# Kernel tuning notes

Hardware: AMD Instinct MI355X
Metric: run time of the kernel (lower is better)

The kernel has to match this reference:

```python
import jax, jax.numpy as jnp
import numpy as np

N_NODES = 50000
N_EDGES = 1600000
IN_CH = 512
HID = 8      # per-head features, layer 1
HEADS = 8
OUT_CH = 40  # num classes
NEG_SLOPE = 0.2  # PyG GATConv default leaky_relu slope


def setup_inputs() -> dict:
    key = jax.random.key(0)
    ks = jax.random.split(key, 8)
    x = jax.random.uniform(ks[0], (N_NODES, IN_CH), dtype=jnp.float32)
    edge_index = jax.random.randint(ks[1], (2, N_EDGES), 0, N_NODES, dtype=jnp.int64)
    s1 = 1.0 / np.sqrt(IN_CH)
    s2 = 1.0 / np.sqrt(HEADS * HID)
    W1 = jax.random.normal(ks[2], (IN_CH, HEADS * HID), dtype=jnp.float32) * s1
    att_src1 = jax.random.normal(ks[3], (HEADS, HID), dtype=jnp.float32) * s2
    att_dst1 = jax.random.normal(ks[4], (HEADS, HID), dtype=jnp.float32) * s2
    b1 = jnp.zeros((HEADS * HID,), dtype=jnp.float32)
    W2 = jax.random.normal(ks[5], (HEADS * HID, OUT_CH), dtype=jnp.float32) * s2
    att_src2 = jax.random.normal(ks[6], (1, OUT_CH), dtype=jnp.float32) * 0.15
    att_dst2 = jax.random.normal(ks[7], (1, OUT_CH), dtype=jnp.float32) * 0.15
    b2 = jnp.zeros((OUT_CH,), dtype=jnp.float32)
    return {"x": x, "edge_index": edge_index, "W1": W1, "att_src1": att_src1,
            "att_dst1": att_dst1, "b1": b1, "W2": W2, "att_src2": att_src2,
            "att_dst2": att_dst2, "b2": b2}


def _row_normalize(x):
    return x / jnp.clip(x.sum(axis=1, keepdims=True), 1e-8, None)


def _gat_conv(x, src, dst, W, att_src, att_dst, bias, heads, out_ch, concat):
    """PyG GATConv (self-loops already included in src/dst)."""
    n = x.shape[0]
    h = (x @ W).reshape(n, heads, out_ch)          # [N, H, C]
    a_src = jnp.sum(h * att_src, axis=-1)          # [N, H]
    a_dst = jnp.sum(h * att_dst, axis=-1)          # [N, H]
    alpha = jax.nn.leaky_relu(a_src[src] + a_dst[dst], NEG_SLOPE)  # [E, H]
    # segment softmax over incoming edges of each dst node
    m = jax.ops.segment_max(alpha, dst, num_segments=n)            # [N, H]
    e = jnp.exp(alpha - m[dst])
    denom = jax.ops.segment_sum(e, dst, num_segments=n)            # [N, H]
    alpha = e / (denom[dst] + 1e-16)
    msg = h[src] * alpha[:, :, None]               # [E, H, C]
    out = jax.ops.segment_sum(msg, dst, num_segments=n)            # [N, H, C]
    out = out.reshape(n, heads * out_ch) if concat else out.mean(axis=1)
    return out + bias


def reference(x, edge_index, W1, att_src1, att_dst1, b1, W2, att_src2, att_dst2, b2):
    n = x.shape[0]
    loops = jnp.arange(n, dtype=edge_index.dtype)
    src = jnp.concatenate([edge_index[0], loops])
    dst = jnp.concatenate([edge_index[1], loops])
    h = _row_normalize(x)
    # dropout omitted: inference mode (training=False)
    h = jax.nn.elu(_gat_conv(h, src, dst, W1, att_src1, att_dst1, b1, HEADS, HID, True))
    return _gat_conv(h, src, dst, W2, att_src2, att_dst2, b2, 1, OUT_CH, False)
```

## Files before the change

### kernel.cpp

```cpp
#include <hip/hip_runtime.h>
#include <math.h>

#define N_NODES 50000
#define IN_CH   512
#define HID     8
#define HEADS   8
#define C1      64
#define OUT_CH  40
#define NEG_SLOPE 0.2f
#define NB      ((N_NODES + 255) / 256)
#define TILE    4096
#define CAP     16384
#define PACKW_BLOCKS 128
#define GEMM1_BLOCKS ((N_NODES + 31) / 32)

__device__ __forceinline__ float leaky(float v) { return fmaxf(v, NEG_SLOPE * v); }
__device__ __forceinline__ float fexp(float v) { return __expf(v); }

typedef __attribute__((ext_vector_type(8))) short short8;
typedef __attribute__((ext_vector_type(4))) short short4v;
typedef __attribute__((ext_vector_type(4))) float f32x4;

__device__ __forceinline__ unsigned short f2bf(float f) {
    unsigned u = __builtin_bit_cast(unsigned, f);
    u += 0x7FFFu + ((u >> 16) & 1u);
    return (unsigned short)(u >> 16);
}
__device__ __forceinline__ float bf2f(unsigned short h) {
    unsigned u = ((unsigned)h) << 16;
    return __builtin_bit_cast(float, u);
}

#define XH_STRIDE_B 272

__global__ __launch_bounds__(256) void k_pre(
    const float* __restrict__ W1, short* __restrict__ bph, short* __restrict__ bpl,
    const int* __restrict__ src, const int* __restrict__ dst, int E,
    int* __restrict__ coarseCur, unsigned int* __restrict__ pairs)
{
    __shared__ int  hist[256];
    __shared__ int  scn[256];
    __shared__ int  offs[256];
    __shared__ unsigned int  pairBuf[TILE];
    __shared__ unsigned char bktBuf[TILE];

    const int t = threadIdx.x;

    if (blockIdx.x < PACKW_BLOCKS) {
        const int idx = blockIdx.x * 256 + t;
        const int k = idx >> 6, col = idx & 63;
        const float w = W1[idx];
        const unsigned short hi = f2bf(w);
        const unsigned short lo = f2bf(w - bf2f(hi));
        const int di = ((k >> 5) * 64 + col) * 32 + (k & 31);
        bph[di] = (short)hi;
        bpl[di] = (short)lo;
        return;
    }

    const int tileBase = (blockIdx.x - PACKW_BLOCKS) * TILE;
    const int n = min(TILE, E - tileBase);

    hist[t] = 0;
    __syncthreads();

    for (int e = t; e < n; e += 256)
        atomicAdd(&hist[dst[tileBase + e] >> 8], 1);
    __syncthreads();

    scn[t] = hist[t];
    __syncthreads();
    #pragma unroll
    for (int off = 1; off < 256; off <<= 1) {
        int xv = (t >= off) ? scn[t - off] : 0;
        __syncthreads();
        scn[t] += xv;
        __syncthreads();
    }

    {
        const int h  = hist[t];
        const int ls = scn[t] - h;
        int off = 0;
        if (h > 0) {
            const int gbase = t * CAP + atomicAdd(&coarseCur[t], h);
            off = gbase - ls;
        }
        offs[t] = off;
        hist[t] = ls;
    }
    __syncthreads();

    for (int e = t; e < n; e += 256) {
        const int s = src[tileBase + e];
        const int d = dst[tileBase + e];
        const int bkt = d >> 8;
        const int pos = atomicAdd(&hist[bkt], 1);
        pairBuf[pos] = (unsigned)s | ((unsigned)(d & 255) << 17);
        bktBuf[pos]  = (unsigned char)bkt;
    }
    __syncthreads();

    for (int i = t; i < n; i += 256)
        pairs[i + offs[bktBuf[i]]] = pairBuf[i];
}

__global__ __launch_bounds__(256) void k_mid(
    const float* __restrict__ x,
    const short* __restrict__ bph, const short* __restrict__ bpl,
    const float* __restrict__ attS, const float* __restrict__ attD,
    unsigned short* __restrict__ h1b, float* __restrict__ aS, float* __restrict__ aD,
    const int* __restrict__ coarseCur, const unsigned int* __restrict__ pairs,
    int* __restrict__ ssrc, int* __restrict__ cumS, int* __restrict__ cumE)
{
    __shared__ unsigned char smem[17536];

    const int tid = threadIdx.x;

    if (blockIdx.x >= GEMM1_BLOCKS) {
        int* hist = (int*)smem;
        int* scn  = hist + 256;
        int* cur  = scn + 256;
        const int b = blockIdx.x - GEMM1_BLOCKS;
        const int t = tid;
        const int dbase = b << 8;
        const int nd = min(256, N_NODES - dbase);
        const int lo = b * CAP;
        const int hi = lo + coarseCur[b];

        hist[t] = 0;
        __syncthreads();
        for (int j = lo + t; j < hi; j += 256)
            atomicAdd(&hist[(pairs[j] >> 17) & 255], 1);
        __syncthreads();

        const int hv = hist[t];
        scn[t] = hv;
        __syncthreads();
        #pragma unroll
        for (int off = 1; off < 256; off <<= 1) {
            int xv = (t >= off) ? scn[t - off] : 0;
            __syncthreads();
            scn[t] += xv;
            __syncthreads();
        }
        if (t < nd) {
            cumS[dbase + t] = lo + scn[t] - hv;
            cumE[dbase + t] = lo + scn[t];
        }
        cur[t] = lo + scn[t] - hv;
        __syncthreads();

        for (int j = lo + t; j < hi; j += 256) {
            const unsigned int p = pairs[j];
            const int pos = atomicAdd(&cur[(p >> 17) & 255], 1);
            ssrc[pos] = (int)(p & 0x1FFFFu);
        }
        return;
    }

    short* xh = (short*)smem;
    short* xl = (short*)(smem + 8704);
    float* rowsum = (float*)(smem + 17408);
    float* houtf  = (float*)smem;

    const int lane = tid & 63;
    const int w    = tid >> 6;
    const int row_off = (w & 1) * 16;
    const int col_off = (w >> 1) * 32;
    const int rowBase = blockIdx.x * 32;

    const int l15 = lane & 15;
    const int kg  = lane >> 4;
    const int a_base = (l15 + row_off) * XH_STRIDE_B + kg * 16;

    const int srow = tid >> 5;
    const int sk4  = tid & 31;

    f32x4 acc0 = {0.f, 0.f, 0.f, 0.f};
    f32x4 acc1 = {0.f, 0.f, 0.f, 0.f};
    float psum[4] = {0.f, 0.f, 0.f, 0.f};
    float4 va[4], vb[4];

    auto LOAD = [&](int c, float4 (&v)[4]) {
        #pragma unroll
        for (int i = 0; i < 4; ++i) {
            const int grow = rowBase + i * 8 + srow;
            v[i] = (grow < N_NODES)
                 ? *(const float4*)(x + (size_t)grow * IN_CH + c * 128 + sk4 * 4)
                 : make_float4(0.f, 0.f, 0.f, 0.f);
        }
    };
    auto STAGE = [&](float4 (&v)[4]) {
        #pragma unroll
        for (int i = 0; i < 4; ++i) {
            const int row = i * 8 + srow;
            const unsigned short h0 = f2bf(v[i].x), h1u = f2bf(v[i].y),
                                 h2 = f2bf(v[i].z), h3  = f2bf(v[i].w);
            short4v hvv = { (short)h0, (short)h1u, (short)h2, (short)h3 };
            short4v lvv = { (short)f2bf(v[i].x - bf2f(h0)), (short)f2bf(v[i].y - bf2f(h1u)),
                            (short)f2bf(v[i].z - bf2f(h2)), (short)f2bf(v[i].w - bf2f(h3)) };
            *(short4v*)((char*)xh + row * XH_STRIDE_B + sk4 * 8) = hvv;
            *(short4v*)((char*)xl + row * XH_STRIDE_B + sk4 * 8) = lvv;
            psum[i] += v[i].x + v[i].y + v[i].z + v[i].w;
        }
    };
    auto MFMA = [&](int c) {
        #pragma unroll
        for (int kk2 = 0; kk2 < 4; ++kk2) {
            const int kk = c * 4 + kk2;
            const short8 ah = *(const short8*)((const char*)xh + a_base + kk2 * 64);
            const short8 al = *(const short8*)((const char*)xl + a_base + kk2 * 64);
            const int b0 = (kk * 64 + col_off + l15) * 32 + kg * 8;
            const int b1 = b0 + 16 * 32;
            const short8 bh0 = *(const short8*)(bph + b0);
            const short8 bl0 = *(const short8*)(bpl + b0);
            const short8 bh1 = *(const short8*)(bph + b1);
            const short8 bl1 = *(const short8*)(bpl + b1);
            acc0 = __builtin_amdgcn_mfma_f32_16x16x32_bf16(ah, bh0, acc0, 0, 0, 0);
            acc1 = __builtin_amdgcn_mfma_f32_16x16x32_bf16(ah, bh1, acc1, 0, 0, 0);
            acc0 = __builtin_amdgcn_mfma_f32_16x16x32_bf16(ah, bl0, acc0, 0, 0, 0);
            acc1 = __builtin_amdgcn_mfma_f32_16x16x32_bf16(ah, bl1, acc1, 0, 0, 0);
            acc0 = __builtin_amdgcn_mfma_f32_16x16x32_bf16(al, bh0, acc0, 0, 0, 0);
            acc1 = __builtin_amdgcn_mfma_f32_16x16x32_bf16(al, bh1, acc1, 0, 0, 0);
        }
    };

    LOAD(0, va);
    STAGE(va);
    __syncthreads();
    LOAD(1, vb);
    MFMA(0);
    __syncthreads();
    STAGE(vb);
    __syncthreads();
    LOAD(2, va);
    MFMA(1);
    __syncthreads();
    STAGE(va);
    __syncthreads();
    LOAD(3, vb);
    MFMA(2);
    __syncthreads();
    STAGE(vb);
    #pragma unroll
    for (int i = 0; i < 4; ++i) {
        float s = psum[i];
        #pragma unroll
        for (int off = 16; off; off >>= 1) s += __shfl_xor(s, off, 32);
        if (sk4 == 0) rowsum[i * 8 + srow] = s;
    }
    __syncthreads();
    MFMA(3);
    __syncthreads();

    #pragma unroll
    for (int r = 0; r < 4; ++r) {
        const int row = row_off + kg * 4 + r;
        const float rs = fmaxf(rowsum[row], 1e-8f);
        houtf[row * 68 + col_off + l15]      = acc0[r] / rs;
        houtf[row * 68 + col_off + 16 + l15] = acc1[r] / rs;
    }
    __syncthreads();

    #pragma unroll
    for (int i = tid; i < 32 * 16; i += 256) {
        const int row = i >> 4, seg = i & 15;
        if (rowBase + row < N_NODES) {
            const float* hs = houtf + row * 68 + seg * 4;
            short4v o = { (short)f2bf(hs[0]), (short)f2bf(hs[1]),
                          (short)f2bf(hs[2]), (short)f2bf(hs[3]) };
            *(short4v*)(h1b + (size_t)(rowBase + row) * 64 + seg * 4) = o;
        }
    }

    {
        const int row = tid >> 3, hd = tid & 7;
        if (rowBase + row < N_NODES) {
            float vs = 0.f, vd = 0.f;
            #pragma unroll
            for (int e2 = 0; e2 < 8; ++e2) {
                const float hv = houtf[row * 68 + hd * 8 + e2];
                vs = fmaf(hv, attS[hd * 8 + e2], vs);
                vd = fmaf(hv, attD[hd * 8 + e2], vd);
            }
            aS[(size_t)(rowBase + row) * 8 + hd] = vs;
            aD[(size_t)(rowBase + row) * 8 + hd] = vd;
        }
    }
}

__global__ __launch_bounds__(256) void k_agg1f(
    const int* __restrict__ cumS, const int* __restrict__ cumE,
    const int* __restrict__ ssrc,
    const float* __restrict__ aS, const float* __restrict__ aD,
    const unsigned short* __restrict__ h1b, const float* __restrict__ b1,
    const float* __restrict__ W2,
    const float* __restrict__ attS2, const float* __restrict__ attD2,
    unsigned short* __restrict__ h2b, float* __restrict__ a2s, float* __restrict__ a2d)
{
    __shared__ float w2s[64 * 40];
    __shared__ float hstage[4][64];

    const int tid  = threadIdx.x;
    const int lane = tid & 63;
    const int w    = tid >> 6;
    const int node = __builtin_amdgcn_readfirstlane(blockIdx.x * 4 + w);
    const int e = lane >> 3;
    const int c = lane & 7;

    #pragma unroll
    for (int i = tid; i < 640; i += 256)
        ((float4*)w2s)[i] = ((const float4*)W2)[i];

    const int start = cumS[node];
    const int end   = cumE[node];

    const float aDn = aD[(size_t)node * 8 + c];
    float acc[8] = {0.f, 0.f, 0.f, 0.f, 0.f, 0.f, 0.f, 0.f};
    float den = 0.f;

    if (e == 0) {
        const float e0 = fexp(leaky(aS[(size_t)node * 8 + c] + aDn));
        const short8 hv = *(const short8*)(h1b + (size_t)node * 64 + c * 8);
        #pragma unroll
        for (int j = 0; j < 8; ++j)
            acc[j] = e0 * bf2f((unsigned short)hv[j]);
        den = e0;
    }

    int base = start;
    for (; base + 32 <= end; base += 32) {
        const int s0 = ssrc[base + e];
        const int s1 = ssrc[base + 8 + e];
        const int s2 = ssrc[base + 16 + e];
        const int s3 = ssrc[base + 24 + e];
        const float aa0 = aS[(size_t)s0 * 8 + c];
        const float aa1 = aS[(size_t)s1 * 8 + c];
        const float aa2 = aS[(size_t)s2 * 8 + c];
        const float aa3 = aS[(size_t)s3 * 8 + c];
        const short8 h0 = *(const short8*)(h1b + ((size_t)s0 << 6) + c * 8);
        const short8 h1v = *(const short8*)(h1b + ((size_t)s1 << 6) + c * 8);
        const short8 h2v = *(const short8*)(h1b + ((size_t)s2 << 6) + c * 8);
        const short8 h3v = *(const short8*)(h1b + ((size_t)s3 << 6) + c * 8);
        const float w0 = fexp(leaky(aa0 + aDn));
        const float w1 = fexp(leaky(aa1 + aDn));
        const float w2 = fexp(leaky(aa2 + aDn));
        const float w3 = fexp(leaky(aa3 + aDn));
        #pragma unroll
        for (int j = 0; j < 8; ++j) {
            acc[j] = fmaf(w0, bf2f((unsigned short)h0[j]), acc[j]);
            acc[j] = fmaf(w1, bf2f((unsigned short)h1v[j]), acc[j]);
            acc[j] = fmaf(w2, bf2f((unsigned short)h2v[j]), acc[j]);
            acc[j] = fmaf(w3, bf2f((unsigned short)h3v[j]), acc[j]);
        }
        den += w0 + w1 + w2 + w3;
    }
    for (; base + 8 <= end; base += 8) {
        const int s = ssrc[base + e];
        const float aa = aS[(size_t)s * 8 + c];
        const short8 hv = *(const short8*)(h1b + ((size_t)s << 6) + c * 8);
        const float wv = fexp(leaky(aa + aDn));
        #pragma unroll
        for (int j = 0; j < 8; ++j)
            acc[j] = fmaf(wv, bf2f((unsigned short)hv[j]), acc[j]);
        den += wv;
    }
    if (base < end) {
        const int nb  = end - base;
        const int idx = base + (e < nb ? e : nb - 1);
        const int s   = ssrc[idx];
        float wv = fexp(leaky(aS[(size_t)s * 8 + c] + aDn));
        if (e >= nb) wv = 0.f;
        const short8 hv = *(const short8*)(h1b + ((size_t)s << 6) + c * 8);
        #pragma unroll
        for (int j = 0; j < 8; ++j)
            acc[j] = fmaf(wv, bf2f((unsigned short)hv[j]), acc[j]);
        den += wv;
    }

    #pragma unroll
    for (int m = 8; m < 64; m <<= 1) {
        den += __shfl_xor(den, m, 64);
        #pragma unroll
        for (int j = 0; j < 8; ++j)
            acc[j] += __shfl_xor(acc[j], m, 64);
    }

    if (e == 0) {
        const float dinv = 1.f / (den + 1e-16f);
        #pragma unroll
        for (int j = 0; j < 8; ++j) {
            const float v = acc[j] * dinv + b1[c * 8 + j];
            hstage[w][c * 8 + j] = v > 0.f ? v : (__expf(v) - 1.f);
        }
    }
    __syncthreads();

    const int j = lane;
    float acc2 = 0.f;
    if (j < OUT_CH) {
        #pragma unroll
        for (int k = 0; k < 64; ++k)
            acc2 = fmaf(hstage[w][k], w2s[k * 40 + j], acc2);
    }
    float vs = (j < OUT_CH) ? acc2 * attS2[j] : 0.f;
    float vd = (j < OUT_CH) ? acc2 * attD2[j] : 0.f;
    #pragma unroll
    for (int off = 32; off; off >>= 1) {
        vs += __shfl_xor(vs, off, 64);
        vd += __shfl_xor(vd, off, 64);
    }
    if (j < OUT_CH) h2b[(size_t)node * 40 + j] = f2bf(acc2);
    if (j == 0) {
        a2s[node] = vs;
        a2d[node] = vd;
    }
}

__global__ __launch_bounds__(256) void k_agg2(
    const int* __restrict__ cumS, const int* __restrict__ cumE,
    const int* __restrict__ ssrc,
    const float* __restrict__ a2s, const float* __restrict__ a2d,
    const unsigned short* __restrict__ h2b, const float* __restrict__ b2,
    float* __restrict__ out)
{
    const int lane = threadIdx.x & 63;
    const int node = __builtin_amdgcn_readfirstlane(blockIdx.x * 4 + (threadIdx.x >> 6));
    const int e = lane >> 3;
    const int c = lane & 7;

    const int start = cumS[node];
    const int end   = cumE[node];

    const float aDd = a2d[node];
    float acc[8] = {0.f, 0.f, 0.f, 0.f, 0.f, 0.f, 0.f, 0.f};
    float den = 0.f;

    if (e == 0) {
        const float e0 = fexp(leaky(a2s[node] + aDd));
        const short8 hv = *(const short8*)(h2b + (size_t)node * 40 + c * 8);
        #pragma unroll
        for (int j = 0; j < 8; ++j)
            acc[j] = e0 * bf2f((unsigned short)hv[j]);
        den = e0;
    }

    int base = start;
    for (; base + 32 <= end; base += 32) {
        const int s0 = ssrc[base + e];
        const int s1 = ssrc[base + 8 + e];
        const int s2 = ssrc[base + 16 + e];
        const int s3 = ssrc[base + 24 + e];
        const float aa0 = a2s[s0];
        const float aa1 = a2s[s1];
        const float aa2 = a2s[s2];
        const float aa3 = a2s[s3];
        const short8 h0 = *(const short8*)(h2b + (size_t)s0 * 40 + c * 8);
        const short8 h1v = *(const short8*)(h2b + (size_t)s1 * 40 + c * 8);
        const short8 h2v = *(const short8*)(h2b + (size_t)s2 * 40 + c * 8);
        const short8 h3v = *(const short8*)(h2b + (size_t)s3 * 40 + c * 8);
        const float w0 = fexp(leaky(aa0 + aDd));
        const float w1 = fexp(leaky(aa1 + aDd));
        const float w2 = fexp(leaky(aa2 + aDd));
        const float w3 = fexp(leaky(aa3 + aDd));
        #pragma unroll
        for (int j = 0; j < 8; ++j) {
            acc[j] = fmaf(w0, bf2f((unsigned short)h0[j]), acc[j]);
            acc[j] = fmaf(w1, bf2f((unsigned short)h1v[j]), acc[j]);
            acc[j] = fmaf(w2, bf2f((unsigned short)h2v[j]), acc[j]);
            acc[j] = fmaf(w3, bf2f((unsigned short)h3v[j]), acc[j]);
        }
        den += w0 + w1 + w2 + w3;
    }
    for (; base + 8 <= end; base += 8) {
        const int s = ssrc[base + e];
        const float aa = a2s[s];
        const short8 hv = *(const short8*)(h2b + (size_t)s * 40 + c * 8);
        const float wv = fexp(leaky(aa + aDd));
        #pragma unroll
        for (int j = 0; j < 8; ++j)
            acc[j] = fmaf(wv, bf2f((unsigned short)hv[j]), acc[j]);
        den += wv;
    }
    if (base < end) {
        const int nb  = end - base;
        const int idx = base + (e < nb ? e : nb - 1);
        const int s   = ssrc[idx];
        float wv = fexp(leaky(a2s[s] + aDd));
        if (e >= nb) wv = 0.f;
        const short8 hv = *(const short8*)(h2b + (size_t)s * 40 + c * 8);
        #pragma unroll
        for (int j = 0; j < 8; ++j)
            acc[j] = fmaf(wv, bf2f((unsigned short)hv[j]), acc[j]);
        den += wv;
    }

    #pragma unroll
    for (int m = 8; m < 64; m <<= 1) {
        den += __shfl_xor(den, m, 64);
        #pragma unroll
        for (int j = 0; j < 8; ++j)
            acc[j] += __shfl_xor(acc[j], m, 64);
    }

    if (e == 0 && c < 5) {
        const float dinv = 1.f / (den + 1e-16f);
        float o[8];
        #pragma unroll
        for (int j = 0; j < 8; ++j)
            o[j] = acc[j] * dinv + b2[c * 8 + j];
        float4* dst0 = (float4*)(out + (size_t)node * OUT_CH + c * 8);
        dst0[0] = make_float4(o[0], o[1], o[2], o[3]);
        dst0[1] = make_float4(o[4], o[5], o[6], o[7]);
    }
}

extern "C" void kernel_launch(void* const* d_in, const int* in_sizes, int n_in,
                              void* d_out, int out_size, void* d_ws, size_t ws_size,
                              hipStream_t stream)
{
    const float* x     = (const float*)d_in[0];
    const int*   ei    = (const int*)d_in[1];
    const float* W1    = (const float*)d_in[2];
    const float* attS1 = (const float*)d_in[3];
    const float* attD1 = (const float*)d_in[4];
    const float* b1    = (const float*)d_in[5];
    const float* W2    = (const float*)d_in[6];
    const float* attS2 = (const float*)d_in[7];
    const float* attD2 = (const float*)d_in[8];
    const float* b2    = (const float*)d_in[9];

    const int E = in_sizes[1] / 2;
    const int* src = ei;
    const int* dst = ei + E;

    float* out = (float*)d_out;
    float* f = (float*)d_ws;
    float* aS1  = f;  f += (size_t)N_NODES * 8;
    float* aD1  = f;  f += (size_t)N_NODES * 8;
    float* a2s  = f;  f += (size_t)N_NODES;
    float* a2d  = f;  f += (size_t)N_NODES;
    unsigned short* h1b = (unsigned short*)f;  f += (size_t)N_NODES * 32;
    unsigned short* h2b = (unsigned short*)f;  f += (size_t)N_NODES * 20 + 64;
    short* bph = (short*)f;  f += 16384;
    short* bpl = (short*)f;  f += 16384;
    unsigned int* pairs = (unsigned int*)f;  f += (size_t)NB * CAP;
    int* ip = (int*)f;
    int* coarseCur = ip;  ip += 256;
    int* cumS      = ip;  ip += N_NODES;
    int* cumE      = ip;  ip += N_NODES;
    int* ssrc      = ip;  ip += (size_t)NB * CAP;

    const int partBlocks = (E + TILE - 1) / TILE;

    hipMemsetAsync(coarseCur, 0, 256 * sizeof(int), stream);

    k_pre<<<PACKW_BLOCKS + partBlocks, 256, 0, stream>>>(W1, bph, bpl,
                                                         src, dst, E, coarseCur, pairs);

    k_mid<<<GEMM1_BLOCKS + NB, 256, 0, stream>>>(x, bph, bpl, attS1, attD1,
                                                 h1b, aS1, aD1,
                                                 coarseCur, pairs, ssrc, cumS, cumE);

    k_agg1f<<<N_NODES / 4, 256, 0, stream>>>(cumS, cumE, ssrc, aS1, aD1, h1b, b1,
                                             W2, attS2, attD2, h2b, a2s, a2d);

    k_agg2<<<N_NODES / 4, 256, 0, stream>>>(cumS, cumE, ssrc, a2s, a2d, h2b, b2, out);
}
```

Before: 171.3 us.

## Load GEMM1 A-operand directly from global into MFMA registers, drop LDS staging

The first-layer GEMM no longer stages x through shared memory as split bf16 hi/lo tiles. Each lane now reads its own 8 contiguous floats per k-step straight from global memory, converts them to hi/lo bf16 in registers and feeds the MFMAs directly. Row sums are reduced with cross-lane shuffles. This removes the LDS writes, LDS reads and several block barriers, and shrinks shared memory use. In exchange, the global loads are 32-byte per-lane strided reads across rows, which coalesce less well than the old row-contiguous float4 pattern, and the software double-buffering is replaced by a plain unrolled loop.

```diff
diff --git a/kernel.cpp b/kernel.cpp
--- a/kernel.cpp
+++ b/kernel.cpp
@@ -31,8 +31,6 @@
     return __builtin_bit_cast(float, u);
 }
 
-#define XH_STRIDE_B 272
-
 __global__ __launch_bounds__(256) void k_pre(
     const float* __restrict__ W1, short* __restrict__ bph, short* __restrict__ bpl,
     const int* __restrict__ src, const int* __restrict__ dst, int E,
@@ -113,12 +111,12 @@
     const int* __restrict__ coarseCur, const unsigned int* __restrict__ pairs,
     int* __restrict__ ssrc, int* __restrict__ cumS, int* __restrict__ cumE)
 {
-    __shared__ unsigned char smem[17536];
+    __shared__ float smemf[32 * 68];
 
     const int tid = threadIdx.x;
 
     if (blockIdx.x >= GEMM1_BLOCKS) {
-        int* hist = (int*)smem;
+        int* hist = (int*)smemf;
         int* scn  = hist + 256;
         int* cur  = scn + 256;
         const int b = blockIdx.x - GEMM1_BLOCKS;
@@ -159,10 +157,7 @@
         return;
     }
 
-    short* xh = (short*)smem;
-    short* xl = (short*)(smem + 8704);
-    float* rowsum = (float*)(smem + 17408);
-    float* houtf  = (float*)smem;
+    float* houtf = smemf;
 
     const int lane = tid & 63;
     const int w    = tid >> 6;
@@ -172,92 +167,53 @@
 
     const int l15 = lane & 15;
     const int kg  = lane >> 4;
-    const int a_base = (l15 + row_off) * XH_STRIDE_B + kg * 16;
-
-    const int srow = tid >> 5;
-    const int sk4  = tid & 31;
+
+    const int myRow = rowBase + row_off + l15;
+    const bool rowOK = (myRow < N_NODES);
+    const float* xrow = x + (size_t)(rowOK ? myRow : 0) * IN_CH + kg * 8;
 
     f32x4 acc0 = {0.f, 0.f, 0.f, 0.f};
     f32x4 acc1 = {0.f, 0.f, 0.f, 0.f};
-    float psum[4] = {0.f, 0.f, 0.f, 0.f};
-    float4 va[4], vb[4];
-
-    auto LOAD = [&](int c, float4 (&v)[4]) {
-        #pragma unroll
-        for (int i = 0; i < 4; ++i) {
-            const int grow = rowBase + i * 8 + srow;
-            v[i] = (grow < N_NODES)
-                 ? *(const float4*)(x + (size_t)grow * IN_CH + c * 128 + sk4 * 4)
-                 : make_float4(0.f, 0.f, 0.f, 0.f);
-        }
-    };
-    auto STAGE = [&](float4 (&v)[4]) {
-        #pragma unroll
-        for (int i = 0; i < 4; ++i) {
-            const int row = i * 8 + srow;
-            const unsigned short h0 = f2bf(v[i].x), h1u = f2bf(v[i].y),
-                                 h2 = f2bf(v[i].z), h3  = f2bf(v[i].w);
-            short4v hvv = { (short)h0, (short)h1u, (short)h2, (short)h3 };
-            short4v lvv = { (short)f2bf(v[i].x - bf2f(h0)), (short)f2bf(v[i].y - bf2f(h1u)),
-                            (short)f2bf(v[i].z - bf2f(h2)), (short)f2bf(v[i].w - bf2f(h3)) };
-            *(short4v*)((char*)xh + row * XH_STRIDE_B + sk4 * 8) = hvv;
-            *(short4v*)((char*)xl + row * XH_STRIDE_B + sk4 * 8) = lvv;
-            psum[i] += v[i].x + v[i].y + v[i].z + v[i].w;
-        }
-    };
-    auto MFMA = [&](int c) {
-        #pragma unroll
-        for (int kk2 = 0; kk2 < 4; ++kk2) {
-            const int kk = c * 4 + kk2;
-            const short8 ah = *(const short8*)((const char*)xh + a_base + kk2 * 64);
-            const short8 al = *(const short8*)((const char*)xl + a_base + kk2 * 64);
-            const int b0 = (kk * 64 + col_off + l15) * 32 + kg * 8;
-            const int b1 = b0 + 16 * 32;
-            const short8 bh0 = *(const short8*)(bph + b0);
-            const short8 bl0 = *(const short8*)(bpl + b0);
-            const short8 bh1 = *(const short8*)(bph + b1);
-            const short8 bl1 = *(const short8*)(bpl + b1);
-            acc0 = __builtin_amdgcn_mfma_f32_16x16x32_bf16(ah, bh0, acc0, 0, 0, 0);
-            acc1 = __builtin_amdgcn_mfma_f32_16x16x32_bf16(ah, bh1, acc1, 0, 0, 0);
-            acc0 = __builtin_amdgcn_mfma_f32_16x16x32_bf16(ah, bl0, acc0, 0, 0, 0);
-            acc1 = __builtin_amdgcn_mfma_f32_16x16x32_bf16(ah, bl1, acc1, 0, 0, 0);
-            acc0 = __builtin_amdgcn_mfma_f32_16x16x32_bf16(al, bh0, acc0, 0, 0, 0);
-            acc1 = __builtin_amdgcn_mfma_f32_16x16x32_bf16(al, bh1, acc1, 0, 0, 0);
-        }
-    };
-
-    LOAD(0, va);
-    STAGE(va);
-    __syncthreads();
-    LOAD(1, vb);
-    MFMA(0);
-    __syncthreads();
-    STAGE(vb);
-    __syncthreads();
-    LOAD(2, va);
-    MFMA(1);
-    __syncthreads();
-    STAGE(va);
-    __syncthreads();
-    LOAD(3, vb);
-    MFMA(2);
-    __syncthreads();
-    STAGE(vb);
-    #pragma unroll
-    for (int i = 0; i < 4; ++i) {
-        float s = psum[i];
-        #pragma unroll
-        for (int off = 16; off; off >>= 1) s += __shfl_xor(s, off, 32);
-        if (sk4 == 0) rowsum[i * 8 + srow] = s;
-    }
-    __syncthreads();
-    MFMA(3);
-    __syncthreads();
+    float psum = 0.f;
+
+    #pragma unroll 4
+    for (int kk = 0; kk < 16; ++kk) {
+        float4 v0 = *(const float4*)(xrow + kk * 32);
+        float4 v1 = *(const float4*)(xrow + kk * 32 + 4);
+        if (!rowOK) {
+            v0 = make_float4(0.f, 0.f, 0.f, 0.f);
+            v1 = make_float4(0.f, 0.f, 0.f, 0.f);
+        }
+        const float vs[8] = {v0.x, v0.y, v0.z, v0.w, v1.x, v1.y, v1.z, v1.w};
+        short8 ah, al;
+        #pragma unroll
+        for (int j = 0; j < 8; ++j) {
+            const unsigned short h = f2bf(vs[j]);
+            ah[j] = (short)h;
+            al[j] = (short)f2bf(vs[j] - bf2f(h));
+            psum += vs[j];
+        }
+        const int b0 = (kk * 64 + col_off + l15) * 32 + kg * 8;
+        const int b1 = b0 + 16 * 32;
+        const short8 bh0 = *(const short8*)(bph + b0);
+        const short8 bl0 = *(const short8*)(bpl + b0);
+        const short8 bh1 = *(const short8*)(bph + b1);
+        const short8 bl1 = *(const short8*)(bpl + b1);
+        acc0 = __builtin_amdgcn_mfma_f32_16x16x32_bf16(ah, bh0, acc0, 0, 0, 0);
+        acc1 = __builtin_amdgcn_mfma_f32_16x16x32_bf16(ah, bh1, acc1, 0, 0, 0);
+        acc0 = __builtin_amdgcn_mfma_f32_16x16x32_bf16(ah, bl0, acc0, 0, 0, 0);
+        acc1 = __builtin_amdgcn_mfma_f32_16x16x32_bf16(ah, bl1, acc1, 0, 0, 0);
+        acc0 = __builtin_amdgcn_mfma_f32_16x16x32_bf16(al, bh0, acc0, 0, 0, 0);
+        acc1 = __builtin_amdgcn_mfma_f32_16x16x32_bf16(al, bh1, acc1, 0, 0, 0);
+    }
+
+    psum += __shfl_xor(psum, 16, 64);
+    psum += __shfl_xor(psum, 32, 64);
 
     #pragma unroll
     for (int r = 0; r < 4; ++r) {
+        const float rs = fmaxf(__shfl(psum, kg * 4 + r, 64), 1e-8f);
         const int row = row_off + kg * 4 + r;
-        const float rs = fmaxf(rowsum[row], 1e-8f);
         houtf[row * 68 + col_off + l15]      = acc0[r] / rs;
         houtf[row * 68 + col_off + 16 + l15] = acc1[r] / rs;
     }
@@ -277,15 +233,15 @@
     {
         const int row = tid >> 3, hd = tid & 7;
         if (rowBase + row < N_NODES) {
-            float vs = 0.f, vd = 0.f;
+            float vsl = 0.f, vdl = 0.f;
             #pragma unroll
             for (int e2 = 0; e2 < 8; ++e2) {
                 const float hv = houtf[row * 68 + hd * 8 + e2];
-                vs = fmaf(hv, attS[hd * 8 + e2], vs);
-                vd = fmaf(hv, attD[hd * 8 + e2], vd);
+                vsl = fmaf(hv, attS[hd * 8 + e2], vsl);
+                vdl = fmaf(hv, attD[hd * 8 + e2], vdl);
             }
-            aS[(size_t)(rowBase + row) * 8 + hd] = vs;
-            aD[(size_t)(rowBase + row) * 8 + hd] = vd;
+            aS[(size_t)(rowBase + row) * 8 + hd] = vsl;
+            aD[(size_t)(rowBase + row) * 8 + hd] = vdl;
         }
     }
 }
```

Result: slower. 179.4 us (+4.8%).
